# Kernel optimization log

Hardware: AMD Instinct MI355X
Metric: run time of the kernel (lower is better)

The kernel has to match this reference:

```python
import jax, jax.numpy as jnp
import numpy as np

N = 100_000   # nodes
E = 1_600_000 # edges
F = 32        # input features
G = 512       # graphs in batch
EPS = 1e-5    # batchnorm eps


def setup_inputs() -> dict:
    key = jax.random.key(0)
    ks = jax.random.split(key, 24)
    d = {
        "x": jax.random.normal(ks[0], (N, F), jnp.float32),
        "edge_index": jax.random.randint(ks[1], (2, E), 0, N),
        "batch": jnp.sort(jax.random.randint(ks[2], (N,), 0, G)),
        "Wl1": jax.random.normal(ks[3], (30, F), jnp.float32) * 0.1,
        "bl1": jax.random.normal(ks[4], (30,), jnp.float32) * 0.1,
        "Wr1": jax.random.normal(ks[5], (30, F), jnp.float32) * 0.1,
        "Wl2": jax.random.normal(ks[6], (30, 30), jnp.float32) * 0.1,
        "bl2": jax.random.normal(ks[7], (30,), jnp.float32) * 0.1,
        "Wr2": jax.random.normal(ks[8], (30, 30), jnp.float32) * 0.1,
        "g1": jax.random.uniform(ks[9], (30,), jnp.float32) + 0.5,
        "b1": jax.random.normal(ks[10], (30,), jnp.float32) * 0.1,
        "m1": jax.random.normal(ks[11], (30,), jnp.float32) * 0.1,
        "v1": jax.random.uniform(ks[12], (30,), jnp.float32) + 0.5,
        "g2": jax.random.uniform(ks[13], (30,), jnp.float32) + 0.5,
        "b2": jax.random.normal(ks[14], (30,), jnp.float32) * 0.1,
        "m2": jax.random.normal(ks[15], (30,), jnp.float32) * 0.1,
        "v2": jax.random.uniform(ks[16], (30,), jnp.float32) + 0.5,
        "W1": jax.random.normal(ks[17], (10, 60), jnp.float32) * 0.1,
        "bb1": jax.random.normal(ks[18], (10,), jnp.float32) * 0.1,
        "W2": jax.random.normal(ks[19], (1, 10), jnp.float32) * 0.1,
        "bb2": jax.random.normal(ks[20], (1,), jnp.float32) * 0.1,
    }
    return d


def reference(x, edge_index, batch, Wl1, bl1, Wr1, Wl2, bl2, Wr2,
              g1, b1, m1, v1, g2, b2, m2, v2, W1, bb1, W2, bb2):
    src, dst = edge_index[0], edge_index[1]

    def sage(h, Wl, bl, Wr):
        # mean aggregation of source features into targets (PyG SAGEConv default)
        s = jax.ops.segment_sum(h[src], dst, num_segments=N)
        cnt = jax.ops.segment_sum(jnp.ones((E,), h.dtype), dst, num_segments=N)
        agg = s / jnp.maximum(cnt, 1.0)[:, None]
        return agg @ Wl.T + bl + h @ Wr.T

    def bn(h, g, b, m, v):  # BatchNorm1d, eval mode (running stats)
        return (h - m) * jax.lax.rsqrt(v + EPS) * g + b

    h = bn(jax.nn.relu(sage(x, Wl1, bl1, Wr1)), g1, b1, m1, v1)
    h = bn(jax.nn.relu(sage(h, Wl2, bl2, Wr2)), g2, b2, m2, v2)

    # dual segment pooling over graphs
    xmax = jax.ops.segment_max(h, batch, num_segments=G)
    xmax = jnp.where(jnp.isfinite(xmax), xmax, 0.0)  # empty graphs -> 0
    s = jax.ops.segment_sum(h, batch, num_segments=G)
    c = jax.ops.segment_sum(jnp.ones((N,), h.dtype), batch, num_segments=G)
    xmean = s / jnp.maximum(c, 1.0)[:, None]

    z = jnp.concatenate([xmax, xmean], axis=1)  # [G, 60]
    z = jax.nn.relu(z @ W1.T + bb1)
    z = z @ W2.T + bb2
    return jax.nn.sigmoid(z)  # [G, 1]
```

## Files before the change

### kernel.cpp

```cpp
#include <hip/hip_runtime.h>
#include <hip/hip_fp16.h>

#define NN 100000
#define NE 1600000
#define FI 32
#define FH 30
#define PAD 32
#define NG 512
#define NBK 782
#define BNODES 128
#define SCB 512
#define CAP 4096
#define NB1 391

__global__ __launch_bounds__(256) void k_bhist(const int* __restrict__ dst, int* __restrict__ bktCnt)
{
    __shared__ int cnt[NBK];
    for (int i = threadIdx.x; i < NBK; i += 256) cnt[i] = 0;
    __syncthreads();
    for (int e = blockIdx.x * 256 + threadIdx.x; e < NE; e += SCB * 256)
        atomicAdd(&cnt[dst[e] >> 7], 1);
    __syncthreads();
    for (int i = threadIdx.x; i < NBK; i += 256) {
        int c = cnt[i];
        if (c) atomicAdd(&bktCnt[i], c);
    }
}

__global__ __launch_bounds__(1024) void k_bscan(const int* __restrict__ bktCnt,
                                                int* __restrict__ bktOff, int* __restrict__ bktPos)
{
    __shared__ int tmp[1024];
    int tid = threadIdx.x;
    int v = (tid < NBK) ? bktCnt[tid] : 0;
    tmp[tid] = v;
    __syncthreads();
    for (int off = 1; off < 1024; off <<= 1) {
        int t = (tid >= off) ? tmp[tid - off] : 0;
        __syncthreads();
        tmp[tid] += t;
        __syncthreads();
    }
    if (tid < NBK) { int ex = tmp[tid] - v; bktOff[tid] = ex; bktPos[tid] = ex; }
    if (tid == 0) bktOff[NBK] = NE;
}

__global__ __launch_bounds__(256) void k_bscatter(const int* __restrict__ src, const int* __restrict__ dst,
                                                  int* __restrict__ bktPos, unsigned* __restrict__ pairs)
{
    __shared__ int cnt[NBK];
    __shared__ int base[NBK];
    for (int i = threadIdx.x; i < NBK; i += 256) cnt[i] = 0;
    __syncthreads();
    for (int e = blockIdx.x * 256 + threadIdx.x; e < NE; e += SCB * 256)
        atomicAdd(&cnt[dst[e] >> 7], 1);
    __syncthreads();
    for (int i = threadIdx.x; i < NBK; i += 256) {
        int c = cnt[i];
        base[i] = c ? atomicAdd(&bktPos[i], c) : 0;
        cnt[i] = 0;
    }
    __syncthreads();
    for (int e = blockIdx.x * 256 + threadIdx.x; e < NE; e += SCB * 256) {
        int d = dst[e];
        int b = d >> 7;
        int r = atomicAdd(&cnt[b], 1);
        pairs[base[b] + r] = ((unsigned)src[e] << 7) | (unsigned)(d & 127);
    }
}

__global__ __launch_bounds__(256) void k_csr(
    const int* __restrict__ bktOff, const unsigned* __restrict__ pairs,
    int* __restrict__ rowstart, int* __restrict__ col)
{
    __shared__ unsigned sp[CAP];
    __shared__ int bins[BNODES], binpos[BNODES], stmp[BNODES];
    int tid = threadIdx.x;
    int bkt = blockIdx.x;
    int gbase = bktOff[bkt];
    int cnt = bktOff[bkt + 1] - gbase;
    if (tid < BNODES) bins[tid] = 0;
    __syncthreads();
    bool inl = (cnt <= CAP);
    if (inl) {
        for (int i = tid; i < cnt; i += 256) {
            unsigned u = pairs[gbase + i];
            sp[i] = u;
            atomicAdd(&bins[u & 127], 1);
        }
    } else {
        for (int i = tid; i < cnt; i += 256)
            atomicAdd(&bins[pairs[gbase + i] & 127], 1);
    }
    __syncthreads();
    if (tid < BNODES) stmp[tid] = bins[tid];
    __syncthreads();
    for (int off = 1; off < BNODES; off <<= 1) {
        int t = 0;
        if (tid < BNODES && tid >= off) t = stmp[tid - off];
        __syncthreads();
        if (tid < BNODES) stmp[tid] += t;
        __syncthreads();
    }
    if (tid < BNODES) {
        int ex = stmp[tid] - bins[tid];
        binpos[tid] = ex;
        int n = (bkt << 7) + tid;
        if (n < NN) rowstart[n] = gbase + ex;
        if (bkt == 0 && tid == 0) rowstart[NN] = NE;
    }
    __syncthreads();
    if (inl) {
        for (int i = tid; i < cnt; i += 256) {
            unsigned u = sp[i];
            int p = atomicAdd(&binpos[u & 127], 1);
            col[gbase + p] = (int)(u >> 7);
        }
    } else {
        for (int i = tid; i < cnt; i += 256) {
            unsigned u = pairs[gbase + i];
            int p = atomicAdd(&binpos[u & 127], 1);
            col[gbase + p] = (int)(u >> 7);
        }
    }
}

__global__ __launch_bounds__(256) void k_tohalf(const float* __restrict__ in, __half2* __restrict__ outp)
{
    int i = blockIdx.x * 256 + threadIdx.x;
    if (i < NN * (PAD / 2)) {
        float2 f = ((const float2*)in)[i];
        outp[i] = __floats2half2_rn(f.x, f.y);
    }
}

__global__ __launch_bounds__(256) void k_aggcsr_h(const int* __restrict__ rowstart,
                                                  const int* __restrict__ col,
                                                  const uint2* __restrict__ hin,
                                                  float* __restrict__ aggout)
{
    int tid = blockIdx.x * 256 + threadIdx.x;
    int n = tid >> 6;
    if (n >= NN) return;
    int lane = threadIdx.x & 63;
    int fb = lane & 7;
    int grp = lane >> 3;
    int rs = rowstart[n], re = rowstart[n + 1];
    float a0 = 0.0f, a1 = 0.0f, a2 = 0.0f, a3 = 0.0f;
    for (int e = rs + grp; e < re; e += 8) {
        uint2 u = hin[(size_t)col[e] * 8 + fb];
        float2 f0 = __half22float2(*(const __half2*)&u.x);
        float2 f1 = __half22float2(*(const __half2*)&u.y);
        a0 += f0.x; a1 += f0.y; a2 += f1.x; a3 += f1.y;
    }
    #pragma unroll
    for (int off = 8; off < 64; off <<= 1) {
        a0 += __shfl_xor(a0, off);
        a1 += __shfl_xor(a1, off);
        a2 += __shfl_xor(a2, off);
        a3 += __shfl_xor(a3, off);
    }
    if (grp == 0) {
        float inv = (re > rs) ? 1.0f / (float)(re - rs) : 0.0f;
        ((float4*)(aggout + (size_t)n * PAD))[fb] =
            make_float4(a0 * inv, a1 * inv, a2 * inv, a3 * inv);
    }
}

__global__ __launch_bounds__(256) void k_t1(
    const float* __restrict__ x, const float* __restrict__ agg,
    const float* __restrict__ Wl, const float* __restrict__ bl, const float* __restrict__ Wr,
    const float* __restrict__ g, const float* __restrict__ b,
    const float* __restrict__ m, const float* __restrict__ v,
    __half2* __restrict__ h1h)
{
    __shared__ float sWl[FH * FI], sWr[FH * FI], sBias[FH], sScale[FH], sShift[FH];
    for (int i = threadIdx.x; i < FH * FI; i += 256) { sWl[i] = Wl[i]; sWr[i] = Wr[i]; }
    if (threadIdx.x < FH) {
        int j = threadIdx.x;
        float sc = g[j] * rsqrtf(v[j] + 1e-5f);
        sBias[j] = bl[j];
        sScale[j] = sc;
        sShift[j] = b[j] - m[j] * sc;
    }
    __syncthreads();
    int n = blockIdx.x * 256 + threadIdx.x;
    if (n >= NN) return;
    float xr[FI], ar[FI];
    #pragma unroll
    for (int k = 0; k < FI; k += 4) {
        float4 xv = *(const float4*)(x + (size_t)n * FI + k);
        float4 av = *(const float4*)(agg + (size_t)n * PAD + k);
        xr[k] = xv.x; xr[k+1] = xv.y; xr[k+2] = xv.z; xr[k+3] = xv.w;
        ar[k] = av.x; ar[k+1] = av.y; ar[k+2] = av.z; ar[k+3] = av.w;
    }
    float res[FH];
    for (int j = 0; j < FH; ++j) {
        float acc = sBias[j];
        #pragma unroll
        for (int k = 0; k < FI; ++k)
            acc += ar[k] * sWl[j * FI + k] + xr[k] * sWr[j * FI + k];
        acc = fmaxf(acc, 0.0f);
        res[j] = acc * sScale[j] + sShift[j];
    }
    __half2* row = h1h + (size_t)n * (PAD / 2);
    #pragma unroll
    for (int j = 0; j < FH; j += 2)
        row[j >> 1] = __floats2half2_rn(res[j], res[j + 1]);
    row[15] = __floats2half2_rn(0.0f, 0.0f);
}

__global__ __launch_bounds__(256) void k_t2(
    const __half2* __restrict__ h1h, const float* agg,
    const float* __restrict__ Wl, const float* __restrict__ bl, const float* __restrict__ Wr,
    const float* __restrict__ g, const float* __restrict__ b,
    const float* __restrict__ m, const float* __restrict__ v,
    float* hout)
{
    __shared__ float sWl[FH * FH], sWr[FH * FH], sBias[FH], sScale[FH], sShift[FH];
    for (int i = threadIdx.x; i < FH * FH; i += 256) { sWl[i] = Wl[i]; sWr[i] = Wr[i]; }
    if (threadIdx.x < FH) {
        int j = threadIdx.x;
        float sc = g[j] * rsqrtf(v[j] + 1e-5f);
        sBias[j] = bl[j];
        sScale[j] = sc;
        sShift[j] = b[j] - m[j] * sc;
    }
    __syncthreads();
    int n = blockIdx.x * 256 + threadIdx.x;
    if (n >= NN) return;
    float xr[FH], ar[FH];
    const __half2* hrow = h1h + (size_t)n * (PAD / 2);
    #pragma unroll
    for (int k2 = 0; k2 < FH / 2; ++k2) {
        float2 fv = __half22float2(hrow[k2]);
        xr[2 * k2] = fv.x; xr[2 * k2 + 1] = fv.y;
    }
    #pragma unroll
    for (int k = 0; k < FH; ++k)
        ar[k] = agg[(size_t)n * PAD + k];
    float res[FH];
    for (int j = 0; j < FH; ++j) {
        float acc = sBias[j];
        #pragma unroll
        for (int k = 0; k < FH; ++k)
            acc += ar[k] * sWl[j * FH + k] + xr[k] * sWr[j * FH + k];
        acc = fmaxf(acc, 0.0f);
        res[j] = acc * sScale[j] + sShift[j];
    }
    #pragma unroll
    for (int j = 0; j < FH; ++j)
        hout[(size_t)n * PAD + j] = res[j];
}

__global__ __launch_bounds__(256) void k_pool(
    const float* __restrict__ h2, const int* __restrict__ batch,
    const float* __restrict__ W1, const float* __restrict__ bb1,
    const float* __restrict__ W2, const float* __restrict__ bb2,
    float* __restrict__ out)
{
    __shared__ float sS[8][FH], sM[8][FH], sz[2 * FH], st[10];
    int tid = threadIdx.x;
    int gi = blockIdx.x;
    int lo = 0, hi = NN;
    while (lo < hi) { int mid = (lo + hi) >> 1; if (batch[mid] < gi) lo = mid + 1; else hi = mid; }
    int start = lo;
    hi = NN;
    while (lo < hi) { int mid = (lo + hi) >> 1; if (batch[mid] <= gi) lo = mid + 1; else hi = mid; }
    int end = lo;

    int f = tid & 31;
    int ng = tid >> 5;
    float sum = 0.0f, mx = -INFINITY;
    if (f < FH) {
        for (int n = start + ng; n < end; n += 8) {
            float val = h2[(size_t)n * PAD + f];
            sum += val;
            mx = fmaxf(mx, val);
        }
        sS[ng][f] = sum;
        sM[ng][f] = mx;
    }
    __syncthreads();
    if (tid < FH) {
        float s = 0.0f, mm = -INFINITY;
        #pragma unroll
        for (int w = 0; w < 8; ++w) { s += sS[w][tid]; mm = fmaxf(mm, sM[w][tid]); }
        int c = end - start;
        sz[tid]      = (c > 0) ? mm : 0.0f;
        sz[FH + tid] = (c > 0) ? s / (float)c : 0.0f;
    }
    __syncthreads();
    if (tid < 10) {
        float t = bb1[tid];
        for (int k = 0; k < 2 * FH; ++k) t += sz[k] * W1[tid * 2 * FH + k];
        st[tid] = fmaxf(t, 0.0f);
    }
    __syncthreads();
    if (tid == 0) {
        float o = bb2[0];
        for (int j = 0; j < 10; ++j) o += st[j] * W2[j];
        out[gi] = 1.0f / (1.0f + expf(-o));
    }
}

extern "C" void kernel_launch(void* const* d_in, const int* in_sizes, int n_in,
                              void* d_out, int out_size, void* d_ws, size_t ws_size,
                              hipStream_t stream)
{
    const float* x   = (const float*)d_in[0];
    const int*   ei  = (const int*)d_in[1];
    const int*   bat = (const int*)d_in[2];
    const float* Wl1 = (const float*)d_in[3];
    const float* bl1 = (const float*)d_in[4];
    const float* Wr1 = (const float*)d_in[5];
    const float* Wl2 = (const float*)d_in[6];
    const float* bl2 = (const float*)d_in[7];
    const float* Wr2 = (const float*)d_in[8];
    const float* g1  = (const float*)d_in[9];
    const float* b1  = (const float*)d_in[10];
    const float* m1  = (const float*)d_in[11];
    const float* v1  = (const float*)d_in[12];
    const float* g2  = (const float*)d_in[13];
    const float* b2  = (const float*)d_in[14];
    const float* m2  = (const float*)d_in[15];
    const float* v2  = (const float*)d_in[16];
    const float* W1  = (const float*)d_in[17];
    const float* bb1 = (const float*)d_in[18];
    const float* W2  = (const float*)d_in[19];
    const float* bb2 = (const float*)d_in[20];

    const int* src = ei;
    const int* dst = ei + NE;

    int* wsi = (int*)d_ws;
    int*      bktCnt   = wsi;
    int*      bktOff   = bktCnt + NBK;
    int*      bktPos   = bktOff + NBK + 2;
    int*      rowstart = bktPos + NBK;
    unsigned* pairs    = (unsigned*)(rowstart + NN + 4);
    int*      col      = (int*)(pairs + NE);
    __half2*  xh       = (__half2*)(col + NE);
    __half2*  h1h      = xh + (size_t)NN * (PAD / 2);
    float*    aggbuf   = (float*)(h1h + (size_t)NN * (PAD / 2));

    hipMemsetAsync(bktCnt, 0, NBK * sizeof(int), stream);

    k_bhist   <<<SCB, 256, 0, stream>>>(dst, bktCnt);
    k_tohalf  <<<(NN * (PAD / 2) + 255) / 256, 256, 0, stream>>>(x, (__half2*)xh);
    k_bscan   <<<1, 1024, 0, stream>>>(bktCnt, bktOff, bktPos);
    k_bscatter<<<SCB, 256, 0, stream>>>(src, dst, bktPos, pairs);
    k_csr     <<<NBK, 256, 0, stream>>>(bktOff, pairs, rowstart, col);

    int ab = (NN * 64 + 255) / 256;
    k_aggcsr_h<<<ab, 256, 0, stream>>>(rowstart, col, (const uint2*)xh, aggbuf);
    k_t1<<<NB1, 256, 0, stream>>>(x, aggbuf, Wl1, bl1, Wr1, g1, b1, m1, v1, h1h);
    k_aggcsr_h<<<ab, 256, 0, stream>>>(rowstart, col, (const uint2*)h1h, aggbuf);
    k_t2<<<NB1, 256, 0, stream>>>(h1h, aggbuf, Wl2, bl2, Wr2, g2, b2, m2, v2, aggbuf);
    k_pool<<<NG, 256, 0, stream>>>(aggbuf, bat, W1, bb1, W2, bb2, (float*)d_out);
}
```

Before: 221.8 us.

## Replace global atomic bucket counting with per-block histograms and hierarchical scan

The bucket sort no longer counts with global atomics and recomputes the histogram inside the scatter kernel. Each block now writes its own partial histogram, and two small kernels compute chunk sums and then per-block exclusive offsets through a two-level scan. The scatter kernel reads its precomputed bases directly, so its duplicate histogram pass and global atomicAdd disappear, and the scatter block count is doubled. In exchange there are two extra kernel launches and about 3 MB of partial-count traffic, and the memset is dropped.

```diff
diff --git a/kernel.cpp b/kernel.cpp
--- a/kernel.cpp
+++ b/kernel.cpp
@@ -9,11 +9,13 @@
 #define NG 512
 #define NBK 782
 #define BNODES 128
-#define SCB 512
+#define SCB 1024
+#define CBLK 32
+#define NCHUNK (SCB / CBLK)
 #define CAP 4096
 #define NB1 391
 
-__global__ __launch_bounds__(256) void k_bhist(const int* __restrict__ dst, int* __restrict__ bktCnt)
+__global__ __launch_bounds__(256) void k_phist(const int* __restrict__ dst, int* __restrict__ partial)
 {
     __shared__ int cnt[NBK];
     for (int i = threadIdx.x; i < NBK; i += 256) cnt[i] = 0;
@@ -21,19 +23,34 @@
     for (int e = blockIdx.x * 256 + threadIdx.x; e < NE; e += SCB * 256)
         atomicAdd(&cnt[dst[e] >> 7], 1);
     __syncthreads();
-    for (int i = threadIdx.x; i < NBK; i += 256) {
-        int c = cnt[i];
-        if (c) atomicAdd(&bktCnt[i], c);
-    }
-}
-
-__global__ __launch_bounds__(1024) void k_bscan(const int* __restrict__ bktCnt,
-                                                int* __restrict__ bktOff, int* __restrict__ bktPos)
+    for (int i = threadIdx.x; i < NBK; i += 256)
+        partial[(size_t)blockIdx.x * NBK + i] = cnt[i];
+}
+
+__global__ __launch_bounds__(256) void k_csum(const int* __restrict__ partial, int* __restrict__ chunksum)
+{
+    int t = blockIdx.x * 256 + threadIdx.x;
+    if (t >= NCHUNK * NBK) return;
+    int c = t / NBK, b = t - c * NBK;
+    int s = 0;
+    #pragma unroll 8
+    for (int k = 0; k < CBLK; ++k)
+        s += partial[(size_t)(c * CBLK + k) * NBK + b];
+    chunksum[c * NBK + b] = s;
+}
+
+__global__ __launch_bounds__(1024) void k_cscan(const int* __restrict__ chunksum,
+                                                int* __restrict__ chunkbase, int* __restrict__ bktOff)
 {
     __shared__ int tmp[1024];
     int tid = threadIdx.x;
-    int v = (tid < NBK) ? bktCnt[tid] : 0;
-    tmp[tid] = v;
+    int cs[NCHUNK];
+    int total = 0;
+    if (tid < NBK) {
+        #pragma unroll
+        for (int c = 0; c < NCHUNK; ++c) { cs[c] = chunksum[c * NBK + tid]; total += cs[c]; }
+    }
+    tmp[tid] = (tid < NBK) ? total : 0;
     __syncthreads();
     for (int off = 1; off < 1024; off <<= 1) {
         int t = (tid >= off) ? tmp[tid - off] : 0;
@@ -41,31 +58,45 @@
         tmp[tid] += t;
         __syncthreads();
     }
-    if (tid < NBK) { int ex = tmp[tid] - v; bktOff[tid] = ex; bktPos[tid] = ex; }
+    if (tid < NBK) {
+        int run = tmp[tid] - total;
+        bktOff[tid] = run;
+        #pragma unroll
+        for (int c = 0; c < NCHUNK; ++c) { chunkbase[c * NBK + tid] = run; run += cs[c]; }
+    }
     if (tid == 0) bktOff[NBK] = NE;
 }
 
-__global__ __launch_bounds__(256) void k_bscatter(const int* __restrict__ src, const int* __restrict__ dst,
-                                                  int* __restrict__ bktPos, unsigned* __restrict__ pairs)
-{
-    __shared__ int cnt[NBK];
-    __shared__ int base[NBK];
-    for (int i = threadIdx.x; i < NBK; i += 256) cnt[i] = 0;
-    __syncthreads();
-    for (int e = blockIdx.x * 256 + threadIdx.x; e < NE; e += SCB * 256)
-        atomicAdd(&cnt[dst[e] >> 7], 1);
-    __syncthreads();
+__global__ __launch_bounds__(256) void k_base(int* __restrict__ partial, const int* __restrict__ chunkbase)
+{
+    int t = blockIdx.x * 256 + threadIdx.x;
+    if (t >= NCHUNK * NBK) return;
+    int c = t / NBK, b = t - c * NBK;
+    int run = chunkbase[c * NBK + b];
+    #pragma unroll 8
+    for (int k = 0; k < CBLK; ++k) {
+        size_t idx = (size_t)(c * CBLK + k) * NBK + b;
+        int v = partial[idx];
+        partial[idx] = run;
+        run += v;
+    }
+}
+
+__global__ __launch_bounds__(256) void k_bscat(const int* __restrict__ src, const int* __restrict__ dst,
+                                               const int* __restrict__ partial, unsigned* __restrict__ pairs)
+{
+    __shared__ int sbase[NBK];
+    __shared__ int scnt[NBK];
     for (int i = threadIdx.x; i < NBK; i += 256) {
-        int c = cnt[i];
-        base[i] = c ? atomicAdd(&bktPos[i], c) : 0;
-        cnt[i] = 0;
+        sbase[i] = partial[(size_t)blockIdx.x * NBK + i];
+        scnt[i] = 0;
     }
     __syncthreads();
     for (int e = blockIdx.x * 256 + threadIdx.x; e < NE; e += SCB * 256) {
         int d = dst[e];
         int b = d >> 7;
-        int r = atomicAdd(&cnt[b], 1);
-        pairs[base[b] + r] = ((unsigned)src[e] << 7) | (unsigned)(d & 127);
+        int r = atomicAdd(&scnt[b], 1);
+        pairs[sbase[b] + r] = ((unsigned)src[e] << 7) | (unsigned)(d & 127);
     }
 }
 
@@ -334,23 +365,26 @@
     const int* dst = ei + NE;
 
     int* wsi = (int*)d_ws;
-    int*      bktCnt   = wsi;
-    int*      bktOff   = bktCnt + NBK;
-    int*      bktPos   = bktOff + NBK + 2;
-    int*      rowstart = bktPos + NBK;
-    unsigned* pairs    = (unsigned*)(rowstart + NN + 4);
-    int*      col      = (int*)(pairs + NE);
-    __half2*  xh       = (__half2*)(col + NE);
-    __half2*  h1h      = xh + (size_t)NN * (PAD / 2);
-    float*    aggbuf   = (float*)(h1h + (size_t)NN * (PAD / 2));
-
-    hipMemsetAsync(bktCnt, 0, NBK * sizeof(int), stream);
-
-    k_bhist   <<<SCB, 256, 0, stream>>>(dst, bktCnt);
-    k_tohalf  <<<(NN * (PAD / 2) + 255) / 256, 256, 0, stream>>>(x, (__half2*)xh);
-    k_bscan   <<<1, 1024, 0, stream>>>(bktCnt, bktOff, bktPos);
-    k_bscatter<<<SCB, 256, 0, stream>>>(src, dst, bktPos, pairs);
-    k_csr     <<<NBK, 256, 0, stream>>>(bktOff, pairs, rowstart, col);
+    int*      partial   = wsi;
+    int*      chunksum  = partial + (size_t)SCB * NBK;
+    int*      chunkbase = chunksum + NCHUNK * NBK;
+    int*      bktOff    = chunkbase + NCHUNK * NBK;
+    int*      rowstart  = bktOff + NBK + 2;
+    unsigned* pairs     = (unsigned*)(rowstart + NN + 4);
+    int*      col       = (int*)(pairs + NE);
+    __half2*  xh        = (__half2*)(col + NE);
+    __half2*  h1h       = xh + (size_t)NN * (PAD / 2);
+    float*    aggbuf    = (float*)(h1h + (size_t)NN * (PAD / 2));
+
+    int pb = (NCHUNK * NBK + 255) / 256;
+
+    k_phist <<<SCB, 256, 0, stream>>>(dst, partial);
+    k_tohalf<<<(NN * (PAD / 2) + 255) / 256, 256, 0, stream>>>(x, (__half2*)xh);
+    k_csum  <<<pb, 256, 0, stream>>>(partial, chunksum);
+    k_cscan <<<1, 1024, 0, stream>>>(chunksum, chunkbase, bktOff);
+    k_base  <<<pb, 256, 0, stream>>>(partial, chunkbase);
+    k_bscat <<<SCB, 256, 0, stream>>>(src, dst, partial, pairs);
+    k_csr   <<<NBK, 256, 0, stream>>>(bktOff, pairs, rowstart, col);
 
     int ab = (NN * 64 + 255) / 256;
     k_aggcsr_h<<<ab, 256, 0, stream>>>(rowstart, col, (const uint2*)xh, aggbuf);
```

New measurement: 202.6 us. 1.09x faster.
